# Optimization experiments

Hardware: AMD Instinct MI355X
Metric: run time of the kernel (lower is better)

The kernel has to match this reference:

```python
import jax, jax.numpy as jnp
import numpy as np

LAT, LONG = 16, 12
C_IN, C_MID = 128, 128
GROUPS = C_IN // 8          # conv groups and GroupNorm groups = 16
E = 200_000                 # number of projection entries (edges)
N = 4096                    # out_size (number of target messages)
PAD = LONG // 2
EPS = 1e-5


def setup_inputs() -> dict:
    key = jax.random.key(0)
    ks = jax.random.split(key, 8)
    x = jax.random.normal(ks[0], (E, C_IN), dtype=jnp.float32)
    proj_index = jax.random.randint(ks[1], (4, E), 0, N * LAT * LONG, dtype=jnp.int64 if jax.config.jax_enable_x64 else jnp.int32)
    proj_delta = jax.random.uniform(ks[2], (4, E), dtype=jnp.float32)
    proj_src_index = jax.random.randint(ks[3], (E,), 0, E, dtype=jnp.int64 if jax.config.jax_enable_x64 else jnp.int32)
    # grouped circular Conv1d: weight [out, in/groups, k] = [128, 2048/16, 12]
    fan_in = (C_IN * LAT // GROUPS) * LONG
    bound = 1.0 / np.sqrt(fan_in)
    conv_w = jax.random.uniform(ks[4], (C_MID, C_IN * LAT // GROUPS, LONG), dtype=jnp.float32, minval=-bound, maxval=bound)
    conv_b = jax.random.uniform(ks[5], (C_MID,), dtype=jnp.float32, minval=-bound, maxval=bound)
    gn_w = jnp.ones((C_MID,), dtype=jnp.float32)
    gn_b = jnp.zeros((C_MID,), dtype=jnp.float32)
    return {"x": x, "out_size": N, "proj_index": proj_index, "proj_delta": proj_delta,
            "proj_src_index": proj_src_index, "conv_w": conv_w, "conv_b": conv_b,
            "gn_w": gn_w, "gn_b": gn_b}


def reference(x, out_size, proj_index, proj_delta, proj_src_index, conv_w, conv_b, gn_w, gn_b):
    # ---- ProjectLatLongSphere: 4 weighted scatter-adds onto the sphere grid ----
    splat = x[proj_src_index]                              # [E, C]
    x_proj = jnp.zeros((out_size * LAT * LONG, C_IN), dtype=x.dtype)
    for i in range(4):                                      # fixed small unroll
        x_proj = x_proj.at[proj_index[i]].add(splat * proj_delta[i][:, None])
    # [N, lat*long, C] -> [N, C, lat*long] -> [N, C*lat, long]
    x_grid = x_proj.reshape(out_size, LAT * LONG, C_IN).transpose(0, 2, 1)
    x_grid = x_grid.reshape(out_size, C_IN * LAT, LONG)

    # ---- grouped circular Conv1d ----
    xp = jnp.concatenate([x_grid[..., -PAD:], x_grid, x_grid[..., :PAD]], axis=-1)  # [N, C*lat, long+2*pad]
    y = jax.lax.conv_general_dilated(
        xp, conv_w, window_strides=(1,), padding='VALID',
        dimension_numbers=('NCH', 'OIH', 'NCH'), feature_group_count=GROUPS)        # [N, C_MID, long+1]
    y = jax.nn.silu(y + conv_b[None, :, None])

    # ---- AvgPool1d(kernel=long) over first `long` positions ----
    y = jnp.mean(y[:, :, :LONG], axis=-1)                   # [N, C_MID]

    # ---- GroupNorm(num_groups=GROUPS) on [N, C_MID] ----
    g = y.reshape(out_size, GROUPS, C_MID // GROUPS)
    mu = jnp.mean(g, axis=-1, keepdims=True)
    var = jnp.var(g, axis=-1, keepdims=True)
    g = (g - mu) * jax.lax.rsqrt(var + EPS)
    return g.reshape(out_size, C_MID) * gn_w + gn_b
```

## Files before the change

### kernel.cpp

```cpp
#include <hip/hip_runtime.h>
#include <hip/hip_fp16.h>
#include <cstdint>

#define LATN 16
#define LONGN 12
#define PP 192
#define CIN 128
#define CMID 128
#define EPSV 1e-5f
#define SPLIT 4
#define CHB 32
#define TST 36
#define UMAXA 4
#define SPN 32

typedef float v2f __attribute__((ext_vector_type(2)));
typedef float f32x4 __attribute__((ext_vector_type(4)));
typedef _Float16 half8 __attribute__((ext_vector_type(8)));


__global__ void count2_kernel(const int* __restrict__ pidx, int* __restrict__ counts,
                              uint2* __restrict__ rec, int E, int padtot, int nthreads) {
    int gid = blockIdx.x * 256 + threadIdx.x;
    uint2 nullrec = make_uint2((uint32_t)PP << 18, 0u);
    for (int j = gid; j < padtot; j += nthreads) rec[j] = nullrec;
    if (gid >= E) return;
#pragma unroll
    for (int i = 0; i < 4; i++) {
        int v = pidx[i * E + gid];
        int n = v / PP;
        int p = v - n * PP;
        atomicAdd(&counts[n * SPN + p / 6], 1);
    }
}

__global__ void scan1_kernel(const int* __restrict__ cnt, int* __restrict__ startp,
                             int* __restrict__ bsum) {
    __shared__ int sd[1024];
    int t = threadIdx.x, b = blockIdx.x;
    int v = (cnt[b * 1024 + t] + 3) & ~3;
    sd[t] = v;
    __syncthreads();
    for (int off = 1; off < 1024; off <<= 1) {
        int x = (t >= off) ? sd[t - off] : 0;
        __syncthreads();
        sd[t] += x;
        __syncthreads();
    }
    startp[b * 1024 + t] = sd[t] - v;
    if (t == 1023) bsum[b] = sd[t];
}

__global__ void scan2_kernel(int* __restrict__ bsum, int* __restrict__ grand, int nb) {
    __shared__ int sd[1024];
    int t = threadIdx.x;
    int v = (t < nb) ? bsum[t] : 0;
    sd[t] = v;
    __syncthreads();
    for (int off = 1; off < 1024; off <<= 1) {
        int x = (t >= off) ? sd[t - off] : 0;
        __syncthreads();
        sd[t] += x;
        __syncthreads();
    }
    if (t < nb) bsum[t] = sd[t] - v;
    if (t == 1023) *grand = sd[1023];
}

__global__ void addback_kernel(int* __restrict__ startp, const int* __restrict__ bsum,
                               int* __restrict__ cur) {
    int v = blockIdx.x * 1024 + threadIdx.x;
    int s = startp[v] + bsum[blockIdx.x];
    startp[v] = s;
    cur[v] = s;
}

__global__ void record_kernel(const int* __restrict__ pidx, const int* __restrict__ src_idx,
                              const float* __restrict__ delta, int* __restrict__ cur,
                              uint2* __restrict__ rec, int E) {
    int e = blockIdx.x * 256 + threadIdx.x;
    if (e >= E) return;
    int src = src_idx[e];
#pragma unroll
    for (int i = 0; i < 4; i++) {
        int v = pidx[i * E + e];
        int n = v / PP;
        int p = v - n * PP;
        int pos = atomicAdd(&cur[n * SPN + p / 6], 1);
        rec[pos] = make_uint2((uint32_t)src | ((uint32_t)p << 18),
                              __float_as_uint(delta[i * E + e]));
    }
}

__global__ void wt2_kernel(const float* __restrict__ w, uint32_t* __restrict__ wt2) {
    int id = blockIdx.x * 256 + threadIdx.x;
    if (id >= CIN * 6 * CMID) return;
    int o = id & 127;
    int kp = (id >> 7) % 6;
    int i = id / (128 * 6);
    float a = w[(o * 128 + i) * 12 + 2 * kp];
    float b = w[(o * 128 + i) * 12 + 2 * kp + 1];
    __half2 h = __floats2half2_rn(a, b);
    wt2[id] = *reinterpret_cast<uint32_t*>(&h);
}


__global__ void wA_kernel(const float* __restrict__ w, _Float16* __restrict__ wA) {
    int id = blockIdx.x * 256 + threadIdx.x;
    if (id >= 16 * 6 * 48 * 64) return;
    int lane = id & 63;
    int rest = id >> 6;
    int s = rest % 48;
    int mt = (rest / 48) % 6;
    int g = rest / (48 * 6);
    int m = mt * 16 + (lane & 15);
    int o = m / 12;
    int t = m - o * 12;
    int og = g * 8 + o;
    _Float16 vals[8];
#pragma unroll
    for (int j = 0; j < 8; j++) {
        int kh = s * 32 + (lane >> 4) * 8 + j;
        int c = kh / PP;
        int p = kh - c * PP;
        int lat = p / LONGN;
        int ll = p - lat * LONGN;
        int k = (ll - t + 18) % 12;
        vals[j] = (_Float16)w[((og)*128 + c * 16 + lat) * 12 + k];
    }
    *(uint4*)(wA + (size_t)id * 8) = *(const uint4*)vals;
}


__global__ __launch_bounds__(256, 5) void scatter_kernel(
    const float* __restrict__ x, const uint2* __restrict__ rec,
    const int* __restrict__ start2, _Float16* __restrict__ grid) {
    __shared__ __align__(16) float tile[(PP + 1) * TST];
    __shared__ int sst[SPN + 1];

    const int bid = blockIdx.x;
    const int n = bid >> 2;
    const int b = bid & 3;
    const int tid = threadIdx.x;

    {
        float4 zz = {0.f, 0.f, 0.f, 0.f};
        float4* t4 = (float4*)tile;
        for (int idx = tid; idx < (PP + 1) * TST / 4; idx += 256) t4[idx] = zz;
        if (tid < SPN + 1) sst[tid] = start2[n * SPN + tid];
    }
    __syncthreads();

    {
        const int il = tid & 7;
        const int slot = tid >> 3;
        const int cbase = b * CHB + il * 4;
        const int e0 = sst[slot];
        const int e1 = sst[slot + 1];
        for (int e = e0; e < e1; e += UMAXA) {
            uint2 rv[UMAXA];
            float4 xv[UMAXA];
#pragma unroll
            for (int u = 0; u < UMAXA; u++) rv[u] = rec[e + u];
#pragma unroll
            for (int u = 0; u < UMAXA; u++) {
                int src = (int)(rv[u].x & 0x3FFFFu);
                xv[u] = *(const float4*)(x + (size_t)src * CIN + cbase);
            }
#pragma unroll
            for (int u = 0; u < UMAXA; u++) {
                float dl = __uint_as_float(rv[u].y);
                int p = (int)(rv[u].x >> 18);
                float* tp = tile + p * TST + (((il + (p & 7)) & 7) << 2);
                float4 t = *(const float4*)tp;
                t.x += xv[u].x * dl;
                t.y += xv[u].y * dl;
                t.z += xv[u].z * dl;
                t.w += xv[u].w * dl;
                *(float4*)tp = t;
            }
        }
    }
    __syncthreads();

    {
        const int c = tid & 31;
        const int pc = tid >> 5;
        const int gch = b * CHB + c;
        _Float16* gdst = grid + ((size_t)n * CIN + gch) * PP;
        const int il = c >> 2;
        const int cm = c & 3;
#pragma unroll
        for (int j16 = 0; j16 < 3; j16++) {
            int pbase = pc * 24 + j16 * 8;
            _Float16 hh[8];
#pragma unroll
            for (int i = 0; i < 8; i++) {
                int p = pbase + i;
                hh[i] = (_Float16)tile[p * TST + ((((il + (p & 7)) & 7) << 2) + cm)];
            }
            *(uint4*)(gdst + pbase) = *(const uint4*)hh;
        }
    }
}


__global__ __launch_bounds__(256, 5) void gemm_kernel(
    const _Float16* __restrict__ grid, const _Float16* __restrict__ wA,
    const float* __restrict__ conv_b, const float* __restrict__ gn_w,
    const float* __restrict__ gn_b, float* __restrict__ out) {
    __shared__ float Clds[96 * 66];

    const int bid = blockIdx.x;
    const int g = bid & 15;
    const int ntile = bid >> 4;
    const int tid = threadIdx.x;
    const int lane = tid & 63;
    const int wv = tid >> 6;
    const int mh = wv & 1;
    const int nh = wv >> 1;

    const int nn = lane & 15;
    const int h = lane >> 4;

    const _Float16* a0 = wA + ((size_t)(g * 6 + mh * 3) * 48) * 512 + lane * 8;
    const _Float16* a1 = a0 + (size_t)48 * 512;
    const _Float16* a2 = a1 + (size_t)48 * 512;
    const _Float16* b0 = grid + ((size_t)(ntile * 64 + nh * 32 + nn) * CIN + g * 8) * PP + h * 8;
    const _Float16* b1 = b0 + (size_t)16 * CIN * PP;

    f32x4 acc00 = {0.f, 0.f, 0.f, 0.f}, acc01 = {0.f, 0.f, 0.f, 0.f};
    f32x4 acc10 = {0.f, 0.f, 0.f, 0.f}, acc11 = {0.f, 0.f, 0.f, 0.f};
    f32x4 acc20 = {0.f, 0.f, 0.f, 0.f}, acc21 = {0.f, 0.f, 0.f, 0.f};

    half8 cA0 = *(const half8*)(a0);
    half8 cA1 = *(const half8*)(a1);
    half8 cA2 = *(const half8*)(a2);
    half8 cB0 = *(const half8*)(b0);
    half8 cB1 = *(const half8*)(b1);

#pragma unroll 4
    for (int s = 0; s < 48; s++) {
        half8 nA0 = cA0, nA1 = cA1, nA2 = cA2, nB0 = cB0, nB1 = cB1;
        if (s + 1 < 48) {
            nA0 = *(const half8*)(a0 + (size_t)(s + 1) * 512);
            nA1 = *(const half8*)(a1 + (size_t)(s + 1) * 512);
            nA2 = *(const half8*)(a2 + (size_t)(s + 1) * 512);
            nB0 = *(const half8*)(b0 + (size_t)(s + 1) * 32);
            nB1 = *(const half8*)(b1 + (size_t)(s + 1) * 32);
        }
        acc00 = __builtin_amdgcn_mfma_f32_16x16x32_f16(cA0, cB0, acc00, 0, 0, 0);
        acc10 = __builtin_amdgcn_mfma_f32_16x16x32_f16(cA1, cB0, acc10, 0, 0, 0);
        acc20 = __builtin_amdgcn_mfma_f32_16x16x32_f16(cA2, cB0, acc20, 0, 0, 0);
        acc01 = __builtin_amdgcn_mfma_f32_16x16x32_f16(cA0, cB1, acc01, 0, 0, 0);
        acc11 = __builtin_amdgcn_mfma_f32_16x16x32_f16(cA1, cB1, acc11, 0, 0, 0);
        acc21 = __builtin_amdgcn_mfma_f32_16x16x32_f16(cA2, cB1, acc21, 0, 0, 0);
        cA0 = nA0; cA1 = nA1; cA2 = nA2; cB0 = nB0; cB1 = nB1;
    }

    {
        const int mbase = mh * 48 + h * 4;
        const int ncol = nh * 32 + nn;
#pragma unroll
        for (int j = 0; j < 4; j++) {
            Clds[(mbase + j) * 66 + ncol] = acc00[j];
            Clds[(mbase + j) * 66 + ncol + 16] = acc01[j];
            Clds[(mbase + 16 + j) * 66 + ncol] = acc10[j];
            Clds[(mbase + 16 + j) * 66 + ncol + 16] = acc11[j];
            Clds[(mbase + 32 + j) * 66 + ncol] = acc20[j];
            Clds[(mbase + 32 + j) * 66 + ncol + 16] = acc21[j];
        }
    }
    __syncthreads();

    {
        const int o = tid & 7;
        const int oc = g * 8 + o;
        const float bias = conv_b[oc];
        const float gw = gn_w[oc], gb = gn_b[oc];
#pragma unroll
        for (int pp = 0; pp < 2; pp++) {
            const int nl = (tid >> 3) + pp * 32;
            float sv = 0.f;
#pragma unroll
            for (int t = 0; t < 12; t++) {
                float z = Clds[(o * 12 + t) * 66 + nl] + bias;
                sv += z / (1.f + __expf(-z));
            }
            sv *= (1.f / 12.f);
            float s1 = sv, s2 = sv * sv;
#pragma unroll
            for (int m = 1; m < 8; m <<= 1) {
                s1 += __shfl_xor(s1, m);
                s2 += __shfl_xor(s2, m);
            }
            float mu = s1 * 0.125f;
            float var = fmaxf(s2 * 0.125f - mu * mu, 0.f);
            float inv = rsqrtf(var + EPSV);
            out[(size_t)(ntile * 64 + nl) * CMID + oc] = (sv - mu) * inv * gw + gb;
        }
    }
}


__global__ __launch_bounds__(256, 5) void fused_kernel(
    const float* __restrict__ x, const uint2* __restrict__ rec,
    const int* __restrict__ start2, const uint32_t* __restrict__ wt2,
    const float* __restrict__ conv_b, const float* __restrict__ gn_w,
    const float* __restrict__ gn_b, float* __restrict__ out) {
    __shared__ __align__(16) float tile[(PP + 1) * TST];
    __shared__ int sst[SPN + 1];

    const int bid = blockIdx.x;
    const int n = bid >> 2;
    const int b = bid & 3;
    const int tid = threadIdx.x;

    {
        float4 zz = {0.f, 0.f, 0.f, 0.f};
        float4* t4 = (float4*)tile;
        for (int idx = tid; idx < (PP + 1) * TST / 4; idx += 256) t4[idx] = zz;
        if (tid < SPN + 1) sst[tid] = start2[n * SPN + tid];
    }
    __syncthreads();

    {
        const int il = tid & 7;
        const int slot = tid >> 3;
        const int cbase = b * CHB + il * 4;
        const int e0 = sst[slot];
        const int e1 = sst[slot + 1];
        float* tbase = tile + il * 4;
        for (int e = e0; e < e1; e += UMAXA) {
            uint2 rv[UMAXA];
            float4 xv[UMAXA];
#pragma unroll
            for (int u = 0; u < UMAXA; u++) rv[u] = rec[e + u];
#pragma unroll
            for (int u = 0; u < UMAXA; u++) {
                int src = (int)(rv[u].x & 0x3FFFFu);
                xv[u] = *(const float4*)(x + (size_t)src * CIN + cbase);
            }
#pragma unroll
            for (int u = 0; u < UMAXA; u++) {
                float dl = __uint_as_float(rv[u].y);
                int p = (int)(rv[u].x >> 18);
                float* tp = tbase + p * TST;
                float4 t = *(const float4*)tp;
                t.x += xv[u].x * dl;
                t.y += xv[u].y * dl;
                t.z += xv[u].z * dl;
                t.w += xv[u].w * dl;
                *(float4*)tp = t;
            }
        }
    }
    __syncthreads();

    const int o_local = tid & 31;
    const int q = tid >> 5;
    const int g_local = o_local >> 3;
    const int o = b * CHB + o_local;
    const int ch = g_local * 8 + q;

    v2f acc2[6];
#pragma unroll
    for (int u = 0; u < 6; u++) acc2[u] = (v2f)(0.f);

    const uint32_t* wcol = wt2 + (size_t)(q * LATN) * 6 * CMID + o;

#pragma unroll
    for (int lat = 0; lat < LATN; lat++) {
        float r[12];
#pragma unroll
        for (int j = 0; j < 12; j++)
            r[j] = tile[(lat * LONGN + j) * TST + ch];
        v2f rp[12];
#pragma unroll
        for (int j = 0; j < 12; j++) {
            rp[j].x = r[(j + 6) % 12];
            rp[j].y = r[(j + 7) % 12];
        }
        const uint32_t* wrow = wcol + (size_t)(lat * 6) * CMID;
#pragma unroll
        for (int kp = 0; kp < 6; kp++) {
            uint32_t wp = wrow[kp * CMID];
            __half2 h2 = *reinterpret_cast<__half2*>(&wp);
            float wlo = __half2float(h2.x);
            float whi = __half2float(h2.y);
            v2f wl2 = {wlo, wlo}, wh2 = {whi, whi};
#pragma unroll
            for (int u = 0; u < 6; u++) {
                acc2[u] += wl2 * rp[(2 * kp + 2 * u) % 12];
                acc2[u] += wh2 * rp[(2 * kp + 2 * u + 1) % 12];
            }
        }
    }
    __syncthreads();

    float* pbuf = tile;
#pragma unroll
    for (int u = 0; u < 6; u++) {
        pbuf[(q * 12 + 2 * u) * 32 + o_local] = acc2[u].x;
        pbuf[(q * 12 + 2 * u + 1) * 32 + o_local] = acc2[u].y;
    }
    __syncthreads();

    float* gbuf = tile + 8 * 12 * 32;
    float sv = 0.f;
    if (tid < 32) {
        float bias = conv_b[b * CHB + tid];
#pragma unroll
        for (int t = 0; t < 12; t++) {
            float z = bias;
#pragma unroll
            for (int qq = 0; qq < 8; qq++) z += pbuf[(qq * 12 + t) * 32 + tid];
            sv += z / (1.f + __expf(-z));
        }
        sv *= (1.f / 12.f);
        gbuf[tid] = sv;
    }
    __syncthreads();
    if (tid < 32) {
        int gb = tid & ~7;
        float mu = 0.f, m2 = 0.f;
#pragma unroll
        for (int j = 0; j < 8; j++) {
            float v = gbuf[gb + j];
            mu += v;
            m2 += v * v;
        }
        mu *= 0.125f;
        float var = m2 * 0.125f - mu * mu;
        var = fmaxf(var, 0.f);
        float inv = rsqrtf(var + EPSV);
        int oc = b * CHB + tid;
        out[(size_t)n * CMID + oc] = (sv - mu) * inv * gn_w[oc] + gn_b[oc];
    }
}

extern "C" void kernel_launch(void* const* d_in, const int* in_sizes, int n_in,
                              void* d_out, int out_size, void* d_ws, size_t ws_size,
                              hipStream_t stream) {
    const float* x = (const float*)d_in[0];
    const int* pidx = (const int*)d_in[2];
    const float* delta = (const float*)d_in[3];
    const int* src_idx = (const int*)d_in[4];
    const float* conv_w = (const float*)d_in[5];
    const float* conv_b = (const float*)d_in[6];
    const float* gn_w = (const float*)d_in[7];
    const float* gn_b = (const float*)d_in[8];
    float* out = (float*)d_out;

    int E = in_sizes[0] / CIN;
    int N = out_size / CMID;
    int nslots = N * SPN;
    int padtot = 4 * E + nslots * 3;

    char* ws = (char*)d_ws;
    size_t off = 0;
    auto alloc = [&](size_t bytes) {
        size_t cur = off;
        off = (off + bytes + 255) & ~(size_t)255;
        return cur;
    };
    int* count2 = (int*)(ws + alloc((size_t)nslots * 4));
    int* start2 = (int*)(ws + alloc((size_t)(nslots + 1) * 4));
    int* bsum   = (int*)(ws + alloc((size_t)1024 * 4));
    uint2* rec  = (uint2*)(ws + alloc((size_t)padtot * 8));
    uint32_t* wt2 = (uint32_t*)(ws + alloc((size_t)CIN * 6 * CMID * 4));
    size_t wA_off = alloc((size_t)16 * 6 * 48 * 64 * 8 * 2);
    size_t grid_off = alloc((size_t)N * CIN * PP * 2);
    _Float16* wA = (_Float16*)(ws + wA_off);
    _Float16* gridbuf = (_Float16*)(ws + grid_off);
    bool two_pass = (off <= ws_size);

    hipMemsetAsync(count2, 0, (size_t)nslots * 4, stream);

    int gE = (E + 255) / 256;
    int nb = nslots / 1024;
    count2_kernel<<<gE, 256, 0, stream>>>(pidx, count2, rec, E, padtot, gE * 256);
    scan1_kernel<<<nb, 1024, 0, stream>>>(count2, start2, bsum);
    scan2_kernel<<<1, 1024, 0, stream>>>(bsum, start2 + nslots, nb);
    addback_kernel<<<nb, 1024, 0, stream>>>(start2, bsum, count2);
    record_kernel<<<gE, 256, 0, stream>>>(pidx, src_idx, delta, count2, rec, E);

    if (two_pass) {
        wA_kernel<<<(16 * 6 * 48 * 64 + 255) / 256, 256, 0, stream>>>(conv_w, wA);
        scatter_kernel<<<N * SPLIT, 256, 0, stream>>>(x, rec, start2, gridbuf);
        gemm_kernel<<<16 * 64, 256, 0, stream>>>(gridbuf, wA, conv_b, gn_w, gn_b, out);
    } else {
        wt2_kernel<<<(CIN * 6 * CMID + 255) / 256, 256, 0, stream>>>(conv_w, wt2);
        fused_kernel<<<N * SPLIT, 256, 0, stream>>>(x, rec, start2, wt2, conv_b, gn_w, gn_b, out);
    }
}
```

Baseline: 289.2 us.

## Double GEMM N-tile per block and fill padding records only in slot tails

The GEMM kernel now computes 128 target messages per block instead of 64, so each wave holds four B fragments and twelve accumulators. This reuses each A (weight) fragment across twice as many MFMAs and halves the grid. The epilogue staging through LDS runs in two passes to fit the existing shared buffer. Separately, the full pre-fill of the record buffer with null records is replaced by a padfill kernel that writes only the unused tail of each slot after record placement. This cuts global writes but adds a launch and raises register pressure, with launch bounds lowered from 5 to 4 blocks per CU.

```diff
diff --git a/kernel.cpp b/kernel.cpp
--- a/kernel.cpp
+++ b/kernel.cpp
@@ -19,15 +19,12 @@
 typedef _Float16 half8 __attribute__((ext_vector_type(8)));
 
 
-__global__ void count2_kernel(const int* __restrict__ pidx, int* __restrict__ counts,
-                              uint2* __restrict__ rec, int E, int padtot, int nthreads) {
-    int gid = blockIdx.x * 256 + threadIdx.x;
-    uint2 nullrec = make_uint2((uint32_t)PP << 18, 0u);
-    for (int j = gid; j < padtot; j += nthreads) rec[j] = nullrec;
-    if (gid >= E) return;
+__global__ void count2_kernel(const int* __restrict__ pidx, int* __restrict__ counts, int E) {
+    int e = blockIdx.x * 256 + threadIdx.x;
+    if (e >= E) return;
 #pragma unroll
     for (int i = 0; i < 4; i++) {
-        int v = pidx[i * E + gid];
+        int v = pidx[i * E + e];
         int n = v / PP;
         int p = v - n * PP;
         atomicAdd(&counts[n * SPN + p / 6], 1);
@@ -90,6 +87,15 @@
         rec[pos] = make_uint2((uint32_t)src | ((uint32_t)p << 18),
                               __float_as_uint(delta[i * E + e]));
     }
+}
+
+__global__ void padfill_kernel(const int* __restrict__ cur, const int* __restrict__ start2,
+                               uint2* __restrict__ rec, int nslots) {
+    int s = blockIdx.x * 256 + threadIdx.x;
+    if (s >= nslots) return;
+    int e = cur[s], e1 = start2[s + 1];
+    uint2 nullrec = make_uint2((uint32_t)PP << 18, 0u);
+    for (; e < e1; ++e) rec[e] = nullrec;
 }
 
 __global__ void wt2_kernel(const float* __restrict__ w, uint32_t* __restrict__ wt2) {
@@ -205,7 +211,7 @@
 }
 
 
-__global__ __launch_bounds__(256, 5) void gemm_kernel(
+__global__ __launch_bounds__(256, 4) void gemm_kernel(
     const _Float16* __restrict__ grid, const _Float16* __restrict__ wA,
     const float* __restrict__ conv_b, const float* __restrict__ gn_w,
     const float* __restrict__ gn_b, float* __restrict__ out) {
@@ -226,28 +232,39 @@
     const _Float16* a0 = wA + ((size_t)(g * 6 + mh * 3) * 48) * 512 + lane * 8;
     const _Float16* a1 = a0 + (size_t)48 * 512;
     const _Float16* a2 = a1 + (size_t)48 * 512;
-    const _Float16* b0 = grid + ((size_t)(ntile * 64 + nh * 32 + nn) * CIN + g * 8) * PP + h * 8;
-    const _Float16* b1 = b0 + (size_t)16 * CIN * PP;
+    const size_t nstride = (size_t)16 * CIN * PP;
+    const _Float16* b0 = grid + ((size_t)(ntile * 128 + nh * 64 + nn) * CIN + g * 8) * PP + h * 8;
+    const _Float16* b1 = b0 + nstride;
+    const _Float16* b2 = b0 + 2 * nstride;
+    const _Float16* b3 = b0 + 3 * nstride;
 
     f32x4 acc00 = {0.f, 0.f, 0.f, 0.f}, acc01 = {0.f, 0.f, 0.f, 0.f};
+    f32x4 acc02 = {0.f, 0.f, 0.f, 0.f}, acc03 = {0.f, 0.f, 0.f, 0.f};
     f32x4 acc10 = {0.f, 0.f, 0.f, 0.f}, acc11 = {0.f, 0.f, 0.f, 0.f};
+    f32x4 acc12 = {0.f, 0.f, 0.f, 0.f}, acc13 = {0.f, 0.f, 0.f, 0.f};
     f32x4 acc20 = {0.f, 0.f, 0.f, 0.f}, acc21 = {0.f, 0.f, 0.f, 0.f};
+    f32x4 acc22 = {0.f, 0.f, 0.f, 0.f}, acc23 = {0.f, 0.f, 0.f, 0.f};
 
     half8 cA0 = *(const half8*)(a0);
     half8 cA1 = *(const half8*)(a1);
     half8 cA2 = *(const half8*)(a2);
     half8 cB0 = *(const half8*)(b0);
     half8 cB1 = *(const half8*)(b1);
+    half8 cB2 = *(const half8*)(b2);
+    half8 cB3 = *(const half8*)(b3);
 
 #pragma unroll 4
     for (int s = 0; s < 48; s++) {
-        half8 nA0 = cA0, nA1 = cA1, nA2 = cA2, nB0 = cB0, nB1 = cB1;
+        half8 nA0 = cA0, nA1 = cA1, nA2 = cA2;
+        half8 nB0 = cB0, nB1 = cB1, nB2 = cB2, nB3 = cB3;
         if (s + 1 < 48) {
             nA0 = *(const half8*)(a0 + (size_t)(s + 1) * 512);
             nA1 = *(const half8*)(a1 + (size_t)(s + 1) * 512);
             nA2 = *(const half8*)(a2 + (size_t)(s + 1) * 512);
             nB0 = *(const half8*)(b0 + (size_t)(s + 1) * 32);
             nB1 = *(const half8*)(b1 + (size_t)(s + 1) * 32);
+            nB2 = *(const half8*)(b2 + (size_t)(s + 1) * 32);
+            nB3 = *(const half8*)(b3 + (size_t)(s + 1) * 32);
         }
         acc00 = __builtin_amdgcn_mfma_f32_16x16x32_f16(cA0, cB0, acc00, 0, 0, 0);
         acc10 = __builtin_amdgcn_mfma_f32_16x16x32_f16(cA1, cB0, acc10, 0, 0, 0);
@@ -255,29 +272,44 @@
         acc01 = __builtin_amdgcn_mfma_f32_16x16x32_f16(cA0, cB1, acc01, 0, 0, 0);
         acc11 = __builtin_amdgcn_mfma_f32_16x16x32_f16(cA1, cB1, acc11, 0, 0, 0);
         acc21 = __builtin_amdgcn_mfma_f32_16x16x32_f16(cA2, cB1, acc21, 0, 0, 0);
-        cA0 = nA0; cA1 = nA1; cA2 = nA2; cB0 = nB0; cB1 = nB1;
-    }
-
-    {
-        const int mbase = mh * 48 + h * 4;
-        const int ncol = nh * 32 + nn;
-#pragma unroll
-        for (int j = 0; j < 4; j++) {
-            Clds[(mbase + j) * 66 + ncol] = acc00[j];
-            Clds[(mbase + j) * 66 + ncol + 16] = acc01[j];
-            Clds[(mbase + 16 + j) * 66 + ncol] = acc10[j];
-            Clds[(mbase + 16 + j) * 66 + ncol + 16] = acc11[j];
-            Clds[(mbase + 32 + j) * 66 + ncol] = acc20[j];
-            Clds[(mbase + 32 + j) * 66 + ncol + 16] = acc21[j];
-        }
-    }
-    __syncthreads();
-
-    {
-        const int o = tid & 7;
-        const int oc = g * 8 + o;
-        const float bias = conv_b[oc];
-        const float gw = gn_w[oc], gb = gn_b[oc];
+        acc02 = __builtin_amdgcn_mfma_f32_16x16x32_f16(cA0, cB2, acc02, 0, 0, 0);
+        acc12 = __builtin_amdgcn_mfma_f32_16x16x32_f16(cA1, cB2, acc12, 0, 0, 0);
+        acc22 = __builtin_amdgcn_mfma_f32_16x16x32_f16(cA2, cB2, acc22, 0, 0, 0);
+        acc03 = __builtin_amdgcn_mfma_f32_16x16x32_f16(cA0, cB3, acc03, 0, 0, 0);
+        acc13 = __builtin_amdgcn_mfma_f32_16x16x32_f16(cA1, cB3, acc13, 0, 0, 0);
+        acc23 = __builtin_amdgcn_mfma_f32_16x16x32_f16(cA2, cB3, acc23, 0, 0, 0);
+        cA0 = nA0; cA1 = nA1; cA2 = nA2;
+        cB0 = nB0; cB1 = nB1; cB2 = nB2; cB3 = nB3;
+    }
+
+    const int o = tid & 7;
+    const int oc = g * 8 + o;
+    const float bias = conv_b[oc];
+    const float gw = gn_w[oc], gb = gn_b[oc];
+
+#pragma unroll
+    for (int half = 0; half < 2; half++) {
+        if (half == 1) __syncthreads();
+        if (nh == half) {
+            const int mbase = mh * 48 + h * 4;
+#pragma unroll
+            for (int j = 0; j < 4; j++) {
+                Clds[(mbase + j) * 66 + nn] = acc00[j];
+                Clds[(mbase + j) * 66 + nn + 16] = acc01[j];
+                Clds[(mbase + j) * 66 + nn + 32] = acc02[j];
+                Clds[(mbase + j) * 66 + nn + 48] = acc03[j];
+                Clds[(mbase + 16 + j) * 66 + nn] = acc10[j];
+                Clds[(mbase + 16 + j) * 66 + nn + 16] = acc11[j];
+                Clds[(mbase + 16 + j) * 66 + nn + 32] = acc12[j];
+                Clds[(mbase + 16 + j) * 66 + nn + 48] = acc13[j];
+                Clds[(mbase + 32 + j) * 66 + nn] = acc20[j];
+                Clds[(mbase + 32 + j) * 66 + nn + 16] = acc21[j];
+                Clds[(mbase + 32 + j) * 66 + nn + 32] = acc22[j];
+                Clds[(mbase + 32 + j) * 66 + nn + 48] = acc23[j];
+            }
+        }
+        __syncthreads();
+
 #pragma unroll
         for (int pp = 0; pp < 2; pp++) {
             const int nl = (tid >> 3) + pp * 32;
@@ -297,7 +329,7 @@
             float mu = s1 * 0.125f;
             float var = fmaxf(s2 * 0.125f - mu * mu, 0.f);
             float inv = rsqrtf(var + EPSV);
-            out[(size_t)(ntile * 64 + nl) * CMID + oc] = (sv - mu) * inv * gw + gb;
+            out[(size_t)(ntile * 128 + half * 64 + nl) * CMID + oc] = (sv - mu) * inv * gw + gb;
         }
     }
 }
@@ -479,16 +511,17 @@
 
     int gE = (E + 255) / 256;
     int nb = nslots / 1024;
-    count2_kernel<<<gE, 256, 0, stream>>>(pidx, count2, rec, E, padtot, gE * 256);
+    count2_kernel<<<gE, 256, 0, stream>>>(pidx, count2, E);
     scan1_kernel<<<nb, 1024, 0, stream>>>(count2, start2, bsum);
     scan2_kernel<<<1, 1024, 0, stream>>>(bsum, start2 + nslots, nb);
     addback_kernel<<<nb, 1024, 0, stream>>>(start2, bsum, count2);
     record_kernel<<<gE, 256, 0, stream>>>(pidx, src_idx, delta, count2, rec, E);
+    padfill_kernel<<<(nslots + 255) / 256, 256, 0, stream>>>(count2, start2, rec, nslots);
 
     if (two_pass) {
         wA_kernel<<<(16 * 6 * 48 * 64 + 255) / 256, 256, 0, stream>>>(conv_w, wA);
         scatter_kernel<<<N * SPLIT, 256, 0, stream>>>(x, rec, start2, gridbuf);
-        gemm_kernel<<<16 * 64, 256, 0, stream>>>(gridbuf, wA, conv_b, gn_w, gn_b, out);
+        gemm_kernel<<<16 * 32, 256, 0, stream>>>(gridbuf, wA, conv_b, gn_w, gn_b, out);
     } else {
         wt2_kernel<<<(CIN * 6 * CMID + 255) / 256, 256, 0, stream>>>(conv_w, wt2);
         fused_kernel<<<N * SPLIT, 256, 0, stream>>>(x, rec, start2, wt2, conv_b, gn_w, gn_b, out);
```

Measured after the change: 302.4 us. +4.5%, slower.

## Store grid in MFMA-fragment layout and fill record padding only in gaps

Applied to the files above, without the earlier changes.

The scatter kernel now writes the fp16 grid in a layout blocked to match the MFMA B-operand fragments: 16 messages by group by k-step with 512-element chunks. Each GEMM k-step then reads a contiguous 1 KB block instead of strided 64-byte pieces spread across messages. Separately, the null-record initialization of the whole padded record buffer is removed from the count kernel. A new padfill kernel writes null records only into the leftover padding slots after record placement. This trades one extra small launch for far fewer stores, and the scatter writes become more scattered.

```diff
diff --git a/kernel.cpp b/kernel.cpp
--- a/kernel.cpp
+++ b/kernel.cpp
@@ -19,15 +19,12 @@
 typedef _Float16 half8 __attribute__((ext_vector_type(8)));
 
 
-__global__ void count2_kernel(const int* __restrict__ pidx, int* __restrict__ counts,
-                              uint2* __restrict__ rec, int E, int padtot, int nthreads) {
-    int gid = blockIdx.x * 256 + threadIdx.x;
-    uint2 nullrec = make_uint2((uint32_t)PP << 18, 0u);
-    for (int j = gid; j < padtot; j += nthreads) rec[j] = nullrec;
-    if (gid >= E) return;
+__global__ void count2_kernel(const int* __restrict__ pidx, int* __restrict__ counts, int E) {
+    int e = blockIdx.x * 256 + threadIdx.x;
+    if (e >= E) return;
 #pragma unroll
     for (int i = 0; i < 4; i++) {
-        int v = pidx[i * E + gid];
+        int v = pidx[i * E + e];
         int n = v / PP;
         int p = v - n * PP;
         atomicAdd(&counts[n * SPN + p / 6], 1);
@@ -90,6 +87,15 @@
         rec[pos] = make_uint2((uint32_t)src | ((uint32_t)p << 18),
                               __float_as_uint(delta[i * E + e]));
     }
+}
+
+__global__ void padfill_kernel(const int* __restrict__ cur, const int* __restrict__ start2,
+                               uint2* __restrict__ rec, int nslots) {
+    int s = blockIdx.x * 256 + threadIdx.x;
+    if (s >= nslots) return;
+    int e = cur[s], e1 = start2[s + 1];
+    uint2 nullrec = make_uint2((uint32_t)PP << 18, 0u);
+    for (; e < e1; ++e) rec[e] = nullrec;
 }
 
 __global__ void wt2_kernel(const float* __restrict__ w, uint32_t* __restrict__ wt2) {
@@ -186,20 +192,24 @@
     {
         const int c = tid & 31;
         const int pc = tid >> 5;
-        const int gch = b * CHB + c;
-        _Float16* gdst = grid + ((size_t)n * CIN + gch) * PP;
+        const int g = b * 4 + (c >> 3);
+        const int cl = c & 7;
         const int il = c >> 2;
         const int cm = c & 3;
+        _Float16* gbase = grid + (((size_t)(n >> 4) * 16 + g) * 48) * 512 + (n & 15) * 32;
 #pragma unroll
         for (int j16 = 0; j16 < 3; j16++) {
             int pbase = pc * 24 + j16 * 8;
+            int k = cl * 192 + pbase;
+            int s = k >> 5;
+            int h = (k >> 3) & 3;
             _Float16 hh[8];
 #pragma unroll
             for (int i = 0; i < 8; i++) {
                 int p = pbase + i;
                 hh[i] = (_Float16)tile[p * TST + ((((il + (p & 7)) & 7) << 2) + cm)];
             }
-            *(uint4*)(gdst + pbase) = *(const uint4*)hh;
+            *(uint4*)(gbase + (size_t)s * 512 + h * 8) = *(const uint4*)hh;
         }
     }
 }
@@ -226,8 +236,12 @@
     const _Float16* a0 = wA + ((size_t)(g * 6 + mh * 3) * 48) * 512 + lane * 8;
     const _Float16* a1 = a0 + (size_t)48 * 512;
     const _Float16* a2 = a1 + (size_t)48 * 512;
-    const _Float16* b0 = grid + ((size_t)(ntile * 64 + nh * 32 + nn) * CIN + g * 8) * PP + h * 8;
-    const _Float16* b1 = b0 + (size_t)16 * CIN * PP;
+
+    const size_t n16stride = (size_t)16 * 48 * 512;
+    const int n16_0 = ntile * 4 + nh * 2;
+    const _Float16* b0 = grid + (size_t)n16_0 * n16stride + (size_t)g * 48 * 512
+                              + nn * 32 + h * 8;
+    const _Float16* b1 = b0 + n16stride;
 
     f32x4 acc00 = {0.f, 0.f, 0.f, 0.f}, acc01 = {0.f, 0.f, 0.f, 0.f};
     f32x4 acc10 = {0.f, 0.f, 0.f, 0.f}, acc11 = {0.f, 0.f, 0.f, 0.f};
@@ -246,8 +260,8 @@
             nA0 = *(const half8*)(a0 + (size_t)(s + 1) * 512);
             nA1 = *(const half8*)(a1 + (size_t)(s + 1) * 512);
             nA2 = *(const half8*)(a2 + (size_t)(s + 1) * 512);
-            nB0 = *(const half8*)(b0 + (size_t)(s + 1) * 32);
-            nB1 = *(const half8*)(b1 + (size_t)(s + 1) * 32);
+            nB0 = *(const half8*)(b0 + (size_t)(s + 1) * 512);
+            nB1 = *(const half8*)(b1 + (size_t)(s + 1) * 512);
         }
         acc00 = __builtin_amdgcn_mfma_f32_16x16x32_f16(cA0, cB0, acc00, 0, 0, 0);
         acc10 = __builtin_amdgcn_mfma_f32_16x16x32_f16(cA1, cB0, acc10, 0, 0, 0);
@@ -479,11 +493,12 @@
 
     int gE = (E + 255) / 256;
     int nb = nslots / 1024;
-    count2_kernel<<<gE, 256, 0, stream>>>(pidx, count2, rec, E, padtot, gE * 256);
+    count2_kernel<<<gE, 256, 0, stream>>>(pidx, count2, E);
     scan1_kernel<<<nb, 1024, 0, stream>>>(count2, start2, bsum);
     scan2_kernel<<<1, 1024, 0, stream>>>(bsum, start2 + nslots, nb);
     addback_kernel<<<nb, 1024, 0, stream>>>(start2, bsum, count2);
     record_kernel<<<gE, 256, 0, stream>>>(pidx, src_idx, delta, count2, rec, E);
+    padfill_kernel<<<(nslots + 255) / 256, 256, 0, stream>>>(count2, start2, rec, nslots);
 
     if (two_pass) {
         wA_kernel<<<(16 * 6 * 48 * 64 + 255) / 256, 256, 0, stream>>>(conv_w, wA);
```

New measurement: 307.9 us. 1.06x slower.
